# Kernel tuning notes

Measured on AMD Instinct MI355X. Metric: run time of the kernel, lower is better.

Reference implementation:

```python
import jax, jax.numpy as jnp
import numpy as np

B, T, D, H, V = 256, 32, 500, 1024, 8000
NF = 512  # conv output channels per window size


def setup_inputs() -> dict:
    key = jax.random.key(0)
    ks = jax.random.split(key, 20)
    s = 0.02
    inp = {
        "text": jax.random.normal(ks[0], (B, T, D), jnp.float32),
        "text_bow": jax.random.uniform(ks[1], (B, V), jnp.float32),
        "text_lengths": jax.random.randint(ks[2], (B,), 1, T + 1).astype(jnp.int32),
        # GRU forward direction (PyTorch layout: [3H, D], [3H, H], gates r,z,n)
        "Wih_f": jax.random.normal(ks[3], (3 * H, D), jnp.float32) * s,
        "Whh_f": jax.random.normal(ks[4], (3 * H, H), jnp.float32) * s,
        "bih_f": jax.random.normal(ks[5], (3 * H,), jnp.float32) * s,
        "bhh_f": jax.random.normal(ks[6], (3 * H,), jnp.float32) * s,
        # GRU backward direction
        "Wih_b": jax.random.normal(ks[7], (3 * H, D), jnp.float32) * s,
        "Whh_b": jax.random.normal(ks[8], (3 * H, H), jnp.float32) * s,
        "bih_b": jax.random.normal(ks[9], (3 * H,), jnp.float32) * s,
        "bhh_b": jax.random.normal(ks[10], (3 * H,), jnp.float32) * s,
        # reduce linear: 2H -> H
        "W_red": jax.random.normal(ks[11], (H, 2 * H), jnp.float32) * s,
        "b_red": jax.random.normal(ks[12], (H,), jnp.float32) * s,
        # conv kernels, reshaped from Conv2d [512,1,ws,2H] to 1D conv [512, 2H, ws]
        "conv_w2": jax.random.normal(ks[13], (NF, 2 * H, 2), jnp.float32) * s,
        "conv_b2": jax.random.normal(ks[14], (NF,), jnp.float32) * s,
        "conv_w3": jax.random.normal(ks[15], (NF, 2 * H, 3), jnp.float32) * s,
        "conv_b3": jax.random.normal(ks[16], (NF,), jnp.float32) * s,
        "conv_w4": jax.random.normal(ks[17], (NF, 2 * H, 4), jnp.float32) * s,
        "conv_b4": jax.random.normal(ks[18], (NF,), jnp.float32) * s,
    }
    return inp


def _run_gru_dir(x, lengths, Wih, Whh, bih, bhh, reverse):
    """One GRU direction over padded [B,T,D] with packed-sequence semantics:
    outputs are zero at t >= length (as pad_packed_sequence produces)."""
    b, t, _ = x.shape
    h_dim = Whh.shape[1]
    xg = jnp.einsum('btd,gd->btg', x, Wih) + bih  # [B,T,3H] input projections
    valid = jnp.arange(t)[None, :] < lengths[:, None]  # [B,T]

    def step(h, inp):
        xg_t, v = inp  # [B,3H], [B]
        hg = h @ Whh.T + bhh
        xr, xz, xn = jnp.split(xg_t, 3, axis=-1)
        hr, hz, hn = jnp.split(hg, 3, axis=-1)
        r = jax.nn.sigmoid(xr + hr)
        z = jax.nn.sigmoid(xz + hz)
        n = jnp.tanh(xn + r * hn)
        h_new = (1.0 - z) * n + z * h
        h_new = jnp.where(v[:, None], h_new, h)
        out = jnp.where(v[:, None], h_new, 0.0)
        return h_new, out

    h0 = jnp.zeros((b, h_dim), x.dtype)
    xs = (jnp.swapaxes(xg, 0, 1), valid.T)  # time-major
    _, outs = jax.lax.scan(step, h0, xs, reverse=reverse)
    return jnp.swapaxes(outs, 0, 1)  # [B,T,H]


def _conv_branch(x_c, w, b, ws):
    # x_c: [B, 2H, T]; w: [512, 2H, ws]; 'same-padding-both-sides' (ws-1) like Conv2d padding=(ws-1,0)
    y = jax.lax.conv_general_dilated(
        x_c, w, window_strides=(1,), padding=[(ws - 1, ws - 1)],
        dimension_numbers=('NCH', 'OIH', 'NCH')) + b[None, :, None]
    y = jax.nn.leaky_relu(y, 0.01)
    return jnp.max(y, axis=-1)  # global max-pool over time -> [B,512]


def reference(text, text_bow, text_lengths, Wih_f, Whh_f, bih_f, bhh_f,
              Wih_b, Whh_b, bih_b, bhh_b, W_red, b_red,
              conv_w2, conv_b2, conv_w3, conv_b3, conv_w4, conv_b4):
    out_f = _run_gru_dir(text, text_lengths, Wih_f, Whh_f, bih_f, bhh_f, reverse=False)
    out_b = _run_gru_dir(text, text_lengths, Wih_b, Whh_b, bih_b, bhh_b, reverse=True)
    gru_init_out = jnp.concatenate([out_f, out_b], axis=-1)  # [B,T,2H]

    # masked mean pooling over valid timesteps (the per-sample Python loop)
    mask = (jnp.arange(gru_init_out.shape[1])[None, :] < text_lengths[:, None]).astype(gru_init_out.dtype)
    gru_mean = jnp.sum(gru_init_out * mask[:, :, None], axis=1) / text_lengths[:, None].astype(gru_init_out.dtype)
    gru_out = gru_mean @ W_red.T + b_red  # [B,H] (dropout is identity at eval)

    x_c = jnp.swapaxes(gru_init_out, 1, 2)  # [B,2H,T]
    con_out = jnp.concatenate([
        _conv_branch(x_c, conv_w2, conv_b2, 2),
        _conv_branch(x_c, conv_w3, conv_b3, 3),
        _conv_branch(x_c, conv_w4, conv_b4, 4),
    ], axis=1)  # [B,1536]

    return jnp.concatenate([gru_out, con_out, text_bow], axis=1)  # [B, H+1536+V]
```

## Files before the change

### kernel.cpp

```cpp
#include <hip/hip_runtime.h>
#include <hip/hip_bf16.h>
#include <math.h>

#define B_ 256
#define T_ 32
#define D_ 500
#define H_ 1024
#define V_ 8000
#define NF_ 512
#define G3H (3*H_)
#define H2 (2*H_)
#define OUTC (H_ + 3*NF_ + V_)
#define KPAD 512
#define NTAP 9
#define NCAT (NTAP*NF_)
#define MS 512
#define WFRAG_G (64*32*512)

typedef float f32x4 __attribute__((ext_vector_type(4)));
typedef short bf16x8 __attribute__((ext_vector_type(8)));

static __device__ __forceinline__ short f2b(float f) {
    unsigned u = __float_as_uint(f);
    unsigned r = (u + 0x7fffu + ((u >> 16) & 1u)) >> 16;
    return (short)r;
}
static __device__ __forceinline__ float b2f(short s) {
    return __uint_as_float(((unsigned)(unsigned short)s) << 16);
}

__global__ __launch_bounds__(256) void gemm_bt(
    const short* __restrict__ A, int lda,
    const short* __restrict__ Bt, int ldb,
    const float* __restrict__ bias,
    void* __restrict__ Cv, int ldc,
    int K, int mode)
{
    __shared__ short As[128 * 32];
    __shared__ short Bs[128 * 32];
    const int tid  = threadIdx.x;
    const int w    = tid >> 6, lane = tid & 63;

    const int nbx = gridDim.x;
    const int nwg = nbx * gridDim.y;
    int flat = blockIdx.y * nbx + blockIdx.x;
    flat = (flat & 7) * (nwg >> 3) + (flat >> 3);
    const int m0 = (flat / nbx) * 128, n0 = (flat % nbx) * 128;

    const int wm   = (w >> 1) * 64, wn = (w & 1) * 64;

    f32x4 acc[4][4];
#pragma unroll
    for (int i = 0; i < 4; ++i)
#pragma unroll
        for (int j = 0; j < 4; ++j) acc[i][j] = (f32x4){0.f, 0.f, 0.f, 0.f};

    const int srow = w * 16 + (lane >> 2);
    const int scol = (lane & 3) * 8;
    const long aoff0 = (long)(m0 + srow) * lda + scol;
    const long aoff1 = (long)(m0 + srow + 64) * lda + scol;
    const long boff0 = (long)(n0 + srow) * ldb + scol;
    const long boff1 = (long)(n0 + srow + 64) * ldb + scol;
    short* lA0 = As + w * 512;        short* lA1 = As + 2048 + w * 512;
    short* lB0 = Bs + w * 512;        short* lB1 = Bs + 2048 + w * 512;

    const int fr = lane & 15, fk = (lane >> 4) * 8;

    for (int kt = 0; kt < K; kt += 32) {
        __builtin_amdgcn_global_load_lds((const __attribute__((address_space(1))) void*)(A + aoff0 + kt),
                                         (__attribute__((address_space(3))) void*)lA0, 16, 0, 0);
        __builtin_amdgcn_global_load_lds((const __attribute__((address_space(1))) void*)(A + aoff1 + kt),
                                         (__attribute__((address_space(3))) void*)lA1, 16, 0, 0);
        __builtin_amdgcn_global_load_lds((const __attribute__((address_space(1))) void*)(Bt + boff0 + kt),
                                         (__attribute__((address_space(3))) void*)lB0, 16, 0, 0);
        __builtin_amdgcn_global_load_lds((const __attribute__((address_space(1))) void*)(Bt + boff1 + kt),
                                         (__attribute__((address_space(3))) void*)lB1, 16, 0, 0);
        __syncthreads();
        bf16x8 af[4], bfv[4];
#pragma unroll
        for (int i = 0; i < 4; ++i) af[i]  = *(const bf16x8*)(As + (wm + i * 16 + fr) * 32 + fk);
#pragma unroll
        for (int j = 0; j < 4; ++j) bfv[j] = *(const bf16x8*)(Bs + (wn + j * 16 + fr) * 32 + fk);
#pragma unroll
        for (int i = 0; i < 4; ++i)
#pragma unroll
            for (int j = 0; j < 4; ++j)
                acc[i][j] = __builtin_amdgcn_mfma_f32_16x16x32_bf16(af[i], bfv[j], acc[i][j], 0, 0, 0);
        __syncthreads();
    }

    const int er = (lane >> 4) * 4;
    const int ec = lane & 15;
#pragma unroll
    for (int i = 0; i < 4; ++i) {
#pragma unroll
        for (int j = 0; j < 4; ++j) {
#pragma unroll
            for (int q = 0; q < 4; ++q) {
                const int m = m0 + wm + i * 16 + er + q;
                const int n = n0 + wn + j * 16 + ec;
                float v = acc[i][j][q];
                if (mode == 0) {
                    ((float*)Cv)[(long)m * ldc + n] = v + bias[n];
                } else if (mode == 2) {
                    ((short*)Cv)[(long)m * ldc + n] = f2b(v + bias[n]);
                } else {
                    ((_Float16*)Cv)[(long)m * ldc + n] = (_Float16)v;
                }
            }
        }
    }
}

__global__ void repack_whh(const float* __restrict__ src, short* __restrict__ dst)
{
    const int idx = blockIdx.x * 256 + threadIdx.x;
    const int l = idx & 63;
    const int kt = (idx >> 6) & 31;
    const int j16 = (idx >> 11) & 63;
    const int g = idx >> 17;
    const long srow = ((long)(g << 10) + (j16 << 4) + (l & 15)) * H_ + kt * 32 + ((l >> 4) << 3);
    short o[8];
#pragma unroll
    for (int e = 0; e < 8; ++e) o[e] = f2b(src[srow + e]);
    *(bf16x8*)&dst[(long)idx * 8] = *(bf16x8*)o;
}

__global__ __launch_bounds__(512) void gru_step_frag(
    const short* __restrict__ hbf_prev, short* __restrict__ hbf_next,
    const float* __restrict__ h32_prev, float* __restrict__ h32_next,
    const short* __restrict__ wfragf, const short* __restrict__ wfragb,
    const float* __restrict__ bhhf, const float* __restrict__ bhhb,
    const short* __restrict__ xgf, const short* __restrict__ xgb,
    short* __restrict__ gout, const int* __restrict__ lengths, int s)
{
    __shared__ f32x4 lacc[4][6][64];
    const int tid = threadIdx.x;
    const int w8 = tid >> 6;
    const int w = w8 & 3;
    const int khalf = w8 >> 2;
    const int lane = tid & 63;
    const int bid = blockIdx.x;
    const int jt = bid & 31;
    const int mtd = bid >> 5;
    const int dir = mtd >> 2, mt = mtd & 3;
    const int m0 = dir * 256 + mt * 64;
    const int j0 = jt * 32;
    const int wm = (w >> 1) * 32, wj = (w & 1) * 16;
    const int tt = dir ? (T_ - 1 - s) : s;

    const short* wfrag = dir ? wfragb : wfragf;
    const float* bhh = dir ? bhhb : bhhf;
    const short* xg  = dir ? xgb : xgf;

    const int fr15 = lane & 15, fk8 = (lane >> 4) * 8;
    const long arow0 = (long)(m0 + wm + fr15) * H_ + fk8 + khalf * 512;
    const long arow1 = arow0 + (long)16 * H_;
    const int j16 = (j0 + wj) >> 4;
    const short* bbase = wfrag + ((long)j16 * 32 + khalf * 16) * 512 + lane * 8;

    f32x4 acc[3][2];
#pragma unroll
    for (int g = 0; g < 3; ++g)
#pragma unroll
        for (int i = 0; i < 2; ++i) acc[g][i] = (f32x4){0.f, 0.f, 0.f, 0.f};

#pragma unroll 4
    for (int kt = 0; kt < 16; ++kt) {
        const bf16x8 af0 = *(const bf16x8*)(hbf_prev + arow0 + kt * 32);
        const bf16x8 af1 = *(const bf16x8*)(hbf_prev + arow1 + kt * 32);
        const bf16x8 b0 = *(const bf16x8*)(bbase + (long)kt * 512);
        const bf16x8 b1 = *(const bf16x8*)(bbase + (long)kt * 512 + WFRAG_G);
        const bf16x8 b2 = *(const bf16x8*)(bbase + (long)kt * 512 + 2 * WFRAG_G);
        acc[0][0] = __builtin_amdgcn_mfma_f32_16x16x32_bf16(af0, b0, acc[0][0], 0, 0, 0);
        acc[0][1] = __builtin_amdgcn_mfma_f32_16x16x32_bf16(af1, b0, acc[0][1], 0, 0, 0);
        acc[1][0] = __builtin_amdgcn_mfma_f32_16x16x32_bf16(af0, b1, acc[1][0], 0, 0, 0);
        acc[1][1] = __builtin_amdgcn_mfma_f32_16x16x32_bf16(af1, b1, acc[1][1], 0, 0, 0);
        acc[2][0] = __builtin_amdgcn_mfma_f32_16x16x32_bf16(af0, b2, acc[2][0], 0, 0, 0);
        acc[2][1] = __builtin_amdgcn_mfma_f32_16x16x32_bf16(af1, b2, acc[2][1], 0, 0, 0);
    }

    if (khalf == 1) {
#pragma unroll
        for (int g = 0; g < 3; ++g)
#pragma unroll
            for (int i = 0; i < 2; ++i)
                lacc[w][g * 2 + i][lane] = acc[g][i];
    }
    __syncthreads();
    if (khalf == 1) return;

#pragma unroll
    for (int g = 0; g < 3; ++g)
#pragma unroll
        for (int i = 0; i < 2; ++i)
            acc[g][i] += lacc[w][g * 2 + i][lane];

    const int er = (lane >> 4) * 4, ec = lane & 15;
    const int jj = j0 + wj + ec;
    const float bhr = bhh[jj], bhz = bhh[H_ + jj], bhn = bhh[2 * H_ + jj];

#pragma unroll
    for (int i = 0; i < 2; ++i) {
#pragma unroll
        for (int q = 0; q < 4; ++q) {
            const int m = m0 + wm + i * 16 + er + q;
            const int b = m & 255;
            const short* xrow = xg + ((long)b * T_ + tt) * G3H;
            const float xr = b2f(xrow[jj]);
            const float xz = b2f(xrow[H_ + jj]);
            const float xn = b2f(xrow[2 * H_ + jj]);
            const float rr = 1.f / (1.f + expf(-(xr + acc[0][i][q] + bhr)));
            const float zz = 1.f / (1.f + expf(-(xz + acc[1][i][q] + bhz)));
            const float nn = tanhf(xn + rr * (acc[2][i][q] + bhn));
            const long hidx = (long)m * H_ + jj;
            const float hp = h32_prev[hidx];
            const float hnew = (1.f - zz) * nn + zz * hp;
            const bool valid = tt < lengths[b];
            const float ho = valid ? hnew : hp;
            h32_next[hidx] = ho;
            hbf_next[hidx] = f2b(ho);
            gout[((long)b * T_ + tt) * H2 + (long)dir * H_ + jj] = valid ? f2b(hnew) : (short)0;
        }
    }
}

__global__ void f2b_pad(const float* __restrict__ src, short* __restrict__ dst,
                        int Ksrc, int Kdst)
{
    const int idx = blockIdx.x * 256 + threadIdx.x;
    const int r = idx / Kdst, c = idx % Kdst;
    dst[idx] = (c < Ksrc) ? f2b(src[(long)r * Ksrc + c]) : (short)0;
}

__global__ void repack_tap(const float* __restrict__ src, short* __restrict__ dst, int ws)
{
    const int idx = blockIdx.x * 256 + threadIdx.x;
    const int rem = idx % (NF_ * H2);
    const int k = idx / (NF_ * H2);
    const int f = rem >> 11, c = rem & 2047;
    dst[idx] = f2b(src[((long)(f << 11) + c) * ws + k]);
}

__global__ void mean_pool2(const short* __restrict__ gin,
                           const int* __restrict__ lengths,
                           short* __restrict__ mean_bf)
{
    const int idx = blockIdx.x * 256 + threadIdx.x;
    const int b = idx >> 11, c = idx & 2047;
    float s = 0.f;
#pragma unroll
    for (int t = 0; t < T_; ++t) s += b2f(gin[((long)(b * T_ + t)) * H2 + c]);
    mean_bf[idx] = f2b(s / (float)lengths[b]);
}

__global__ void conv_max(const _Float16* __restrict__ P,
                         const float* __restrict__ cb2, const float* __restrict__ cb3,
                         const float* __restrict__ cb4, float* __restrict__ out)
{
    const int idx = blockIdx.x * 256 + threadIdx.x;
    const int b = idx / 1536, u0 = idx % 1536;
    int Tout, ws, base, f; float bias;
    if (u0 < 512)       { ws = 2; Tout = 33; base = 0;    f = u0;        bias = cb2[f]; }
    else if (u0 < 1024) { ws = 3; Tout = 34; base = 1024; f = u0 - 512;  bias = cb3[f]; }
    else                { ws = 4; Tout = 35; base = 2560; f = u0 - 1024; bias = cb4[f]; }
    const _Float16* Pb = P + (long)b * T_ * NCAT + base + f;
    float m = -INFINITY;
    for (int u = 0; u < Tout; ++u) {
        float s = bias;
        for (int k = 0; k < ws; ++k) {
            const int t = u - (ws - 1) + k;
            if (t >= 0 && t < T_) s += (float)Pb[(long)t * NCAT + k * NF_];
        }
        s = s > 0.f ? s : 0.01f * s;
        m = fmaxf(m, s);
    }
    out[(long)b * OUTC + H_ + u0] = m;
}

__global__ void bow_copy(const float* __restrict__ bow, float* __restrict__ out)
{
    const int idx = blockIdx.x * 256 + threadIdx.x;
    const int b = idx / 2000, q = idx % 2000;
    const float4* src = (const float4*)(bow + (long)b * V_);
    float4* dst = (float4*)(out + (long)b * OUTC + H_ + 3 * NF_);
    dst[q] = src[q];
}

extern "C" void kernel_launch(void* const* d_in, const int* in_sizes, int n_in,
                              void* d_out, int out_size, void* d_ws, size_t ws_size,
                              hipStream_t stream)
{
    const float* text    = (const float*)d_in[0];
    const float* bow     = (const float*)d_in[1];
    const int*   lengths = (const int*)  d_in[2];
    const float* Wih_f   = (const float*)d_in[3];
    const float* Whh_f   = (const float*)d_in[4];
    const float* bih_f   = (const float*)d_in[5];
    const float* bhh_f   = (const float*)d_in[6];
    const float* Wih_b   = (const float*)d_in[7];
    const float* Whh_b   = (const float*)d_in[8];
    const float* bih_b   = (const float*)d_in[9];
    const float* bhh_b   = (const float*)d_in[10];
    const float* W_red   = (const float*)d_in[11];
    const float* b_red   = (const float*)d_in[12];
    const float* cw2     = (const float*)d_in[13];
    const float* cb2     = (const float*)d_in[14];
    const float* cw3     = (const float*)d_in[15];
    const float* cb3     = (const float*)d_in[16];
    const float* cw4     = (const float*)d_in[17];
    const float* cb4     = (const float*)d_in[18];
    float* out = (float*)d_out;

    char* ws = (char*)d_ws;
    size_t off = 0;
    short* xg_f = (short*)(ws + off); off += (size_t)B_ * T_ * G3H * 2;
    short* xg_b = (short*)(ws + off); off += (size_t)B_ * T_ * G3H * 2;
    _Float16* P    = (_Float16*)(char*)xg_f;
    short* wtap_bf = (short*)((char*)xg_f + (size_t)B_ * T_ * NCAT * 2);
    short* gin_bf = (short*)(ws + off); off += (size_t)B_ * T_ * H2 * 2;
    short* text_bf = gin_bf;
    short* wihf_bf = (short*)((char*)gin_bf + (size_t)B_ * T_ * KPAD * 2);
    short* wihb_bf = wihf_bf + (size_t)G3H * KPAD;
    short* wfragf  = (short*)(ws + off); off += (size_t)3 * WFRAG_G * 2;
    short* wfragb  = (short*)(ws + off); off += (size_t)3 * WFRAG_G * 2;
    short* wred_bf = (short*)(ws + off); off += (size_t)H_ * H2 * 2;
    float* h32     = (float*)(ws + off); off += (size_t)2 * MS * H_ * 4;
    short* h_bf    = (short*)(ws + off); off += (size_t)2 * MS * H_ * 2;
    short* gmean_bf= (short*)(ws + off); off += (size_t)B_ * H2 * 2;

    const dim3 blk(256);

    f2b_pad<<<dim3((B_ * T_ * KPAD) / 256), blk, 0, stream>>>(text, text_bf, D_, KPAD);
    f2b_pad<<<dim3((G3H * KPAD) / 256), blk, 0, stream>>>(Wih_f, wihf_bf, D_, KPAD);
    f2b_pad<<<dim3((G3H * KPAD) / 256), blk, 0, stream>>>(Wih_b, wihb_bf, D_, KPAD);
    f2b_pad<<<dim3((H_ * H2) / 256), blk, 0, stream>>>(W_red, wred_bf, H2, H2);
    repack_whh<<<dim3(1536), blk, 0, stream>>>(Whh_f, wfragf);
    repack_whh<<<dim3(1536), blk, 0, stream>>>(Whh_b, wfragb);

    gemm_bt<<<dim3(G3H / 128, (B_ * T_) / 128), blk, 0, stream>>>(
        text_bf, KPAD, wihf_bf, KPAD, bih_f, xg_f, G3H, KPAD, 2);
    gemm_bt<<<dim3(G3H / 128, (B_ * T_) / 128), blk, 0, stream>>>(
        text_bf, KPAD, wihb_bf, KPAD, bih_b, xg_b, G3H, KPAD, 2);

    hipMemsetAsync(h32, 0, (size_t)MS * H_ * 4, stream);
    hipMemsetAsync(h_bf, 0, (size_t)MS * H_ * 2, stream);
    for (int s = 0; s < T_; ++s) {
        const int cur = s & 1, nxt = (s + 1) & 1;
        gru_step_frag<<<dim3(256), dim3(512), 0, stream>>>(
            h_bf + (size_t)cur * MS * H_, h_bf + (size_t)nxt * MS * H_,
            h32 + (size_t)cur * MS * H_, h32 + (size_t)nxt * MS * H_,
            wfragf, wfragb, bhh_f, bhh_b, xg_f, xg_b,
            gin_bf, lengths, s);
    }

    mean_pool2<<<dim3((B_ * H2) / 256), blk, 0, stream>>>(gin_bf, lengths, gmean_bf);
    gemm_bt<<<dim3(H_ / 128, B_ / 128), blk, 0, stream>>>(
        gmean_bf, H2, wred_bf, H2, b_red, out, OUTC, H2, 0);

    repack_tap<<<dim3((2 * NF_ * H2) / 256), blk, 0, stream>>>(cw2, wtap_bf, 2);
    repack_tap<<<dim3((3 * NF_ * H2) / 256), blk, 0, stream>>>(cw3, wtap_bf + (size_t)2 * NF_ * H2, 3);
    repack_tap<<<dim3((4 * NF_ * H2) / 256), blk, 0, stream>>>(cw4, wtap_bf + (size_t)5 * NF_ * H2, 4);
    gemm_bt<<<dim3(NCAT / 128, (B_ * T_) / 128), blk, 0, stream>>>(
        gin_bf, H2, wtap_bf, H2, nullptr, P, NCAT, H2, 3);

    conv_max<<<dim3((B_ * 1536) / 256), blk, 0, stream>>>(P, cb2, cb3, cb4, out);
    bow_copy<<<dim3((B_ * 2000) / 256), blk, 0, stream>>>(bow, out);
}
```

Measured before the change: 1.035 ms.

## Split GRU step recurrent GEMM into four K-quarters across 1024-thread blocks

Each GRU timestep block now uses 16 waves instead of 8, and the K dimension of the recurrent h·Whh product is split four ways instead of two. Each block now covers 32 rows by 64 hidden units, where it used to cover 64 rows by 32 units. Partial sums from three K-quarters go through a larger LDS buffer and are reduced by the first wave group before the gate epilogue. The aim is more parallel waves per step to hide latency on the latency-bound sequential loop. The cost is a larger LDS reduction, more idle waves during the epilogue, and possible register pressure at 1024 threads.

```diff
diff --git a/kernel.cpp b/kernel.cpp
--- a/kernel.cpp
+++ b/kernel.cpp
@@ -126,7 +126,7 @@
     *(bf16x8*)&dst[(long)idx * 8] = *(bf16x8*)o;
 }
 
-__global__ __launch_bounds__(512) void gru_step_frag(
+__global__ __launch_bounds__(1024) void gru_step_frag(
     const short* __restrict__ hbf_prev, short* __restrict__ hbf_next,
     const float* __restrict__ h32_prev, float* __restrict__ h32_next,
     const short* __restrict__ wfragf, const short* __restrict__ wfragb,
@@ -134,19 +134,18 @@
     const short* __restrict__ xgf, const short* __restrict__ xgb,
     short* __restrict__ gout, const int* __restrict__ lengths, int s)
 {
-    __shared__ f32x4 lacc[4][6][64];
+    __shared__ f32x4 lacc[3][4][6][64];
     const int tid = threadIdx.x;
-    const int w8 = tid >> 6;
-    const int w = w8 & 3;
-    const int khalf = w8 >> 2;
+    const int w16 = tid >> 6;
+    const int jw = w16 & 3;
+    const int kq = w16 >> 2;
     const int lane = tid & 63;
     const int bid = blockIdx.x;
-    const int jt = bid & 31;
-    const int mtd = bid >> 5;
-    const int dir = mtd >> 2, mt = mtd & 3;
-    const int m0 = dir * 256 + mt * 64;
-    const int j0 = jt * 32;
-    const int wm = (w >> 1) * 32, wj = (w & 1) * 16;
+    const int jt4 = bid & 15;
+    const int mg = bid >> 4;
+    const int dir = mg >> 3;
+    const int m0 = mg * 32;
+    const int j0 = jt4 * 64;
     const int tt = dir ? (T_ - 1 - s) : s;
 
     const short* wfrag = dir ? wfragb : wfragf;
@@ -154,10 +153,10 @@
     const short* xg  = dir ? xgb : xgf;
 
     const int fr15 = lane & 15, fk8 = (lane >> 4) * 8;
-    const long arow0 = (long)(m0 + wm + fr15) * H_ + fk8 + khalf * 512;
+    const long arow0 = (long)(m0 + fr15) * H_ + fk8 + kq * 256;
     const long arow1 = arow0 + (long)16 * H_;
-    const int j16 = (j0 + wj) >> 4;
-    const short* bbase = wfrag + ((long)j16 * 32 + khalf * 16) * 512 + lane * 8;
+    const int j16 = jt4 * 4 + jw;
+    const short* bbase = wfrag + ((long)j16 * 32 + kq * 8) * 512 + lane * 8;
 
     f32x4 acc[3][2];
 #pragma unroll
@@ -165,8 +164,8 @@
 #pragma unroll
         for (int i = 0; i < 2; ++i) acc[g][i] = (f32x4){0.f, 0.f, 0.f, 0.f};
 
-#pragma unroll 4
-    for (int kt = 0; kt < 16; ++kt) {
+#pragma unroll
+    for (int kt = 0; kt < 8; ++kt) {
         const bf16x8 af0 = *(const bf16x8*)(hbf_prev + arow0 + kt * 32);
         const bf16x8 af1 = *(const bf16x8*)(hbf_prev + arow1 + kt * 32);
         const bf16x8 b0 = *(const bf16x8*)(bbase + (long)kt * 512);
@@ -180,31 +179,33 @@
         acc[2][1] = __builtin_amdgcn_mfma_f32_16x16x32_bf16(af1, b2, acc[2][1], 0, 0, 0);
     }
 
-    if (khalf == 1) {
+    if (kq >= 1) {
 #pragma unroll
         for (int g = 0; g < 3; ++g)
 #pragma unroll
             for (int i = 0; i < 2; ++i)
-                lacc[w][g * 2 + i][lane] = acc[g][i];
+                lacc[kq - 1][jw][g * 2 + i][lane] = acc[g][i];
     }
     __syncthreads();
-    if (khalf == 1) return;
-
-#pragma unroll
-    for (int g = 0; g < 3; ++g)
-#pragma unroll
-        for (int i = 0; i < 2; ++i)
-            acc[g][i] += lacc[w][g * 2 + i][lane];
+    if (kq >= 1) return;
+
+#pragma unroll
+    for (int p = 0; p < 3; ++p)
+#pragma unroll
+        for (int g = 0; g < 3; ++g)
+#pragma unroll
+            for (int i = 0; i < 2; ++i)
+                acc[g][i] += lacc[p][jw][g * 2 + i][lane];
 
     const int er = (lane >> 4) * 4, ec = lane & 15;
-    const int jj = j0 + wj + ec;
+    const int jj = j0 + jw * 16 + ec;
     const float bhr = bhh[jj], bhz = bhh[H_ + jj], bhn = bhh[2 * H_ + jj];
 
 #pragma unroll
     for (int i = 0; i < 2; ++i) {
 #pragma unroll
         for (int q = 0; q < 4; ++q) {
-            const int m = m0 + wm + i * 16 + er + q;
+            const int m = m0 + i * 16 + er + q;
             const int b = m & 255;
             const short* xrow = xg + ((long)b * T_ + tt) * G3H;
             const float xr = b2f(xrow[jj]);
@@ -347,7 +348,7 @@
     hipMemsetAsync(h_bf, 0, (size_t)MS * H_ * 2, stream);
     for (int s = 0; s < T_; ++s) {
         const int cur = s & 1, nxt = (s + 1) & 1;
-        gru_step_frag<<<dim3(256), dim3(512), 0, stream>>>(
+        gru_step_frag<<<dim3(256), dim3(1024), 0, stream>>>(
             h_bf + (size_t)cur * MS * H_, h_bf + (size_t)nxt * MS * H_,
             h32 + (size_t)cur * MS * H_, h32 + (size_t)nxt * MS * H_,
             wfragf, wfragb, bhh_f, bhh_b, xg_f, xg_b,
```

Measured after the change: 1.036 ms. Within noise of the previous version (+0.1%).
